# Kernel optimization log

Measured on AMD Instinct MI355X. Metric: run time of the kernel, lower is better.

Reference implementation:

```python
import jax, jax.numpy as jnp
import numpy as np

N, E, G = 50000, 1600000, 64
XDIM, HID, NF, NG, GDIM, NL = 32, 128, 128, 50, 16, 6
CUTOFF = 10.0
SHID = 64
EPS = 1e-5

_offset = jnp.linspace(0.0, CUTOFF, NG)
_coeff = -0.5 / float((CUTOFF / (NG - 1)) ** 2)


def _bn(h, g, b):
    m = h.mean(axis=0)
    v = h.var(axis=0)
    return (h - m) * jax.lax.rsqrt(v + EPS) * g + b


def setup_inputs() -> dict:
    key = jax.random.key(0)
    ks = jax.random.split(key, 48)

    def w(k, shape):
        fan = shape[-2] if len(shape) >= 2 else shape[-1]
        return (jax.random.normal(k, shape, jnp.float32) / np.sqrt(fan)).astype(jnp.float32)

    inp = {
        "x": jax.random.normal(ks[0], (N, XDIM), jnp.float32),
        "edge_index": jax.random.randint(ks[1], (2, E), 0, N, dtype=jnp.int32).astype(jnp.int64),
        "edge_attr": jax.random.normal(ks[2], (E, 3), jnp.float32),
        "batch": jnp.sort(jax.random.randint(ks[3], (N,), 0, G, dtype=jnp.int32)).astype(jnp.int64),
        "u": jax.random.normal(ks[4], (G, GDIM), jnp.float32),
        # node encoder MLP: lin -> bn -> relu -> lin
        "We1": w(ks[5], (XDIM, HID)), "be1": jnp.zeros(HID), "ge1": jnp.ones(HID), "bte1": jnp.zeros(HID),
        "We2": w(ks[6], (HID, HID)), "be2": jnp.zeros(HID),
        # 6 stacked interactions
        "Wf1": w(ks[7], (NL, NG, NF)), "bf1": jnp.zeros((NL, NF)),
        "Wf2": w(ks[8], (NL, NF, NF)), "bf2": jnp.zeros((NL, NF)),
        "Wd1": w(ks[9], (NL, HID, HID)), "bd1": jnp.zeros((NL, HID)),
        "Wd2": w(ks[10], (NL, HID, HID)), "bd2": jnp.zeros((NL, HID)),
        # global MLP: lin -> bn -> relu -> lin
        "Wg1": w(ks[11], (GDIM, HID)), "bg1": jnp.zeros(HID), "gg1": jnp.ones(HID), "btg1": jnp.zeros(HID),
        "Wg2": w(ks[12], (HID, HID)), "bg2": jnp.zeros(HID),
        # shift predictor: [2*HID, 64, 64, 1]
        "Ws1": w(ks[13], (2 * HID, SHID)), "bs1": jnp.zeros(SHID), "gs1": jnp.ones(SHID), "bts1": jnp.zeros(SHID),
        "Ws2": w(ks[14], (SHID, SHID)), "bs2": jnp.zeros(SHID), "gs2": jnp.ones(SHID), "bts2": jnp.zeros(SHID),
        "Ws3": w(ks[15], (SHID, 1)), "bs3": jnp.zeros(1),
    }
    return inp


def reference(x, edge_index, edge_attr, batch, u,
              We1, be1, ge1, bte1, We2, be2,
              Wf1, bf1, Wf2, bf2, Wd1, bd1, Wd2, bd2,
              Wg1, bg1, gg1, btg1, Wg2, bg2,
              Ws1, bs1, gs1, bts1, Ws2, bs2, gs2, bts2, Ws3, bs3):
    row = edge_index[0]  # source j
    col = edge_index[1]  # target i

    # node encoder
    h = jax.nn.relu(_bn(x @ We1 + be1, ge1, bte1)) @ We2 + be2  # [N,HID]

    # gaussian smearing of edge lengths
    d = jnp.linalg.norm(edge_attr, axis=1)  # [E]
    ea = jnp.exp(_coeff * jnp.square(d[:, None] - _offset[None, :]))  # [E,NG]

    for l in range(NL):
        W = jax.nn.relu(ea @ Wf1[l] + bf1[l]) @ Wf2[l] + bf2[l]  # [E,NF]
        msg = h[row] * W                                          # gather + elementwise
        agg = jax.ops.segment_sum(msg, col, num_segments=N)       # scatter-add
        h = h + (jax.nn.relu(agg @ Wd1[l] + bd1[l]) @ Wd2[l] + bd2[l])

    # global MLP
    u_p = jax.nn.relu(_bn(u @ Wg1 + bg1, gg1, btg1)) @ Wg2 + bg2  # [G,HID]

    # shift predictor on [h, u_p[batch]]
    s = jnp.concatenate([h, u_p[batch]], axis=1)  # [N,2*HID]
    s = jax.nn.relu(_bn(s @ Ws1 + bs1, gs1, bts1))
    s = jax.nn.relu(_bn(s @ Ws2 + bs2, gs2, bts2))
    shifts = s @ Ws3 + bs3  # [N,1]
    return shifts, h, ea, u_p
```

## Files before the change

kernel.cpp:

```cpp
#include <hip/hip_runtime.h>

#define NN 50000
#define NE 1600000
#define NGR 64
#define XD 32
#define HID 128
#define NF 128
#define NG 50
#define GD 16
#define NL 6
#define SH 64
#define EPSF 1e-5f
#define TBL 4096
#define INVSTEP 320.0f

typedef __bf16 bf16_t;
typedef bf16_t bf16x8 __attribute__((ext_vector_type(8)));
typedef float f32x4 __attribute__((ext_vector_type(4)));

__device__ __forceinline__ unsigned pack_bf2(float a, float b) {
  unsigned short ua = __builtin_bit_cast(unsigned short, (bf16_t)a);
  unsigned short ub = __builtin_bit_cast(unsigned short, (bf16_t)b);
  return (unsigned)ua | ((unsigned)ub << 16);
}

__global__ __launch_bounds__(256) void k_hist(const int* __restrict__ col,
                                              int* __restrict__ hist) {
  for (int e = blockIdx.x * 256 + threadIdx.x; e < NE; e += gridDim.x * 256)
    atomicAdd(&hist[col[e]], 1);
}

__global__ __launch_bounds__(1024) void k_scan(int* __restrict__ hist,
                                               int* __restrict__ rowptr) {
  const int tid = threadIdx.x;
  const int CH = 49;
  const int base = tid * CH;
  int s = 0;
  for (int i = 0; i < CH; ++i) {
    int idx = base + i;
    if (idx < NN) s += hist[idx];
  }
  __shared__ int part[1024];
  part[tid] = s;
  __syncthreads();
  for (int off = 1; off < 1024; off <<= 1) {
    int v = (tid >= off) ? part[tid - off] : 0;
    __syncthreads();
    part[tid] += v;
    __syncthreads();
  }
  int run = part[tid] - s;
  for (int i = 0; i < CH; ++i) {
    int idx = base + i;
    if (idx < NN) {
      int c = hist[idx];
      rowptr[idx] = run;
      hist[idx] = run;
      run += c;
    }
  }
  if (tid == 0) rowptr[NN] = NE;
}

__global__ __launch_bounds__(256) void k_scatter2(const int* __restrict__ col,
    const int* __restrict__ row, const float* __restrict__ eattr,
    int* __restrict__ cursor, int4* __restrict__ metap) {
  for (int e = blockIdx.x * 256 + threadIdx.x; e < NE; e += gridDim.x * 256) {
    float ax = eattr[(size_t)e * 3], ay = eattr[(size_t)e * 3 + 1], az = eattr[(size_t)e * 3 + 2];
    float d = sqrtf(ax * ax + ay * ay + az * az);
    float tt = fminf(d * INVSTEP, (float)(TBL - 2) + 0.999f);
    int id = (int)tt;
    int c = col[e];
    int pos = atomicAdd(&cursor[c], 1);
    metap[pos] = make_int4(id, __float_as_int(tt - (float)id), row[e], c);
  }
}

__global__ __launch_bounds__(128) void k_tabbuild3(
    const float* __restrict__ Wf1, const float* __restrict__ bf1,
    const float* __restrict__ Wf2, const float* __restrict__ bf2,
    unsigned int* __restrict__ tabp) {
  const int bid = blockIdx.x;
  const int l = bid / (TBL / 8);
  const int t0 = (bid - l * (TBL / 8)) * 8;
  const int c = threadIdx.x;
  __shared__ float g_s[9][NG];
  __shared__ float f1_s[9][NF];
  for (int i = c; i < 9 * NG; i += 128) {
    int kk = i / NG, g = i - kk * NG;
    int t = min(t0 + kk, TBL - 1);
    float d = (float)t * (1.0f / INVSTEP);
    float z = d - 0.2040816327f * (float)g;
    g_s[kk][g] = expf(-12.005f * z * z);
  }
  __syncthreads();
  const float* W1 = Wf1 + (size_t)l * NG * NF;
  float f1r[9];
#pragma unroll
  for (int kk = 0; kk < 9; ++kk) f1r[kk] = bf1[(size_t)l * NF + c];
  for (int g = 0; g < NG; ++g) {
    float w = W1[g * NF + c];
#pragma unroll
    for (int kk = 0; kk < 9; ++kk) f1r[kk] = fmaf(g_s[kk][g], w, f1r[kk]);
  }
#pragma unroll
  for (int kk = 0; kk < 9; ++kk) f1_s[kk][c] = fmaxf(f1r[kk], 0.f);
  __syncthreads();
  const float* W2 = Wf2 + (size_t)l * NF * NF;
  float outr[9];
#pragma unroll
  for (int kk = 0; kk < 9; ++kk) outr[kk] = bf2[(size_t)l * NF + c];
  for (int k = 0; k < NF; ++k) {
    float w = W2[k * NF + c];
#pragma unroll
    for (int kk = 0; kk < 9; ++kk) outr[kk] = fmaf(f1_s[kk][k], w, outr[kk]);
  }
#pragma unroll
  for (int kk = 0; kk < 8; ++kk)
    tabp[((size_t)l * TBL + t0 + kk) * NF + c] = pack_bf2(outr[kk], outr[kk + 1]);
}

__global__ __launch_bounds__(256) void k_prepw(const float* __restrict__ Wd1,
    const float* __restrict__ Wd2,
    bf16_t* __restrict__ Wd1Thi, bf16_t* __restrict__ Wd1Tlo,
    bf16_t* __restrict__ Wd2Thi, bf16_t* __restrict__ Wd2Tlo) {
  const int S1 = NL * 128 * 128;
  int idx = blockIdx.x * 256 + threadIdx.x;
  if (idx < 2 * S1) {
    int which = idx / S1;
    int jj = idx - which * S1;
    int l = jj / (128 * 128);
    int r = jj - l * (128 * 128);
    int c = r >> 7, k = r & 127;
    const float* W = (which == 0) ? Wd1 : Wd2;
    float v = W[(size_t)l * 128 * 128 + (size_t)k * 128 + c];
    bf16_t hv = (bf16_t)v;
    bf16_t lv = (bf16_t)(v - (float)hv);
    if (which == 0) { Wd1Thi[jj] = hv; Wd1Tlo[jj] = lv; }
    else            { Wd2Thi[jj] = hv; Wd2Tlo[jj] = lv; }
  }
}

__global__ __launch_bounds__(256) void k_enc1(const float* __restrict__ x,
    const float* __restrict__ We1, const float* __restrict__ be1,
    float* __restrict__ t, float* __restrict__ stats) {
  int c = threadIdx.x & 127;
  int half = threadIdx.x >> 7;
  float b = be1[c];
  float psum = 0.f, psq = 0.f;
  for (int n = blockIdx.x * 2 + half; n < NN; n += gridDim.x * 2) {
    const float* xr = x + (size_t)n * XD;
    float v = b;
#pragma unroll
    for (int k = 0; k < XD; ++k) v = fmaf(xr[k], We1[k * HID + c], v);
    t[(size_t)n * HID + c] = v;
    psum += v; psq += v * v;
  }
  __shared__ float s0[256], s1[256];
  s0[threadIdx.x] = psum; s1[threadIdx.x] = psq;
  __syncthreads();
  if (threadIdx.x < 128) {
    atomicAdd(&stats[threadIdx.x], s0[threadIdx.x] + s0[threadIdx.x + 128]);
    atomicAdd(&stats[128 + threadIdx.x], s1[threadIdx.x] + s1[threadIdx.x + 128]);
  }
}

__global__ __launch_bounds__(128) void k_bn_fin(const float* __restrict__ gamma,
    const float* __restrict__ beta, float* __restrict__ stats, int C, float invn) {
  int c = threadIdx.x;
  if (c < C) {
    float mean = stats[c] * invn;
    float var = stats[128 + c] * invn - mean * mean;
    float a = gamma[c] * rsqrtf(var + EPSF);
    stats[256 + c] = a;
    stats[384 + c] = beta[c] - mean * a;
  }
}

__global__ __launch_bounds__(128) void k_enc2(const float* __restrict__ t,
    const float* __restrict__ stats, const float* __restrict__ We2,
    const float* __restrict__ be2, float* __restrict__ h,
    unsigned int* __restrict__ hbf) {
  __shared__ float r[HID];
  int c = threadIdx.x;
  float a = stats[256 + c], b = stats[384 + c];
  float bias = be2[c];
  for (int n = blockIdx.x; n < NN; n += gridDim.x) {
    float v = fmaf(t[(size_t)n * HID + c], a, b);
    r[c] = fmaxf(v, 0.f);
    __syncthreads();
    float acc = bias;
#pragma unroll 8
    for (int k = 0; k < HID; ++k) acc = fmaf(r[k], We2[k * HID + c], acc);
    h[(size_t)n * HID + c] = acc;
    float o = __shfl_down(acc, 1);
    if ((c & 1) == 0) hbf[(size_t)n * 64 + (c >> 1)] = pack_bf2(acc, o);
    __syncthreads();
  }
}

__global__ __launch_bounds__(256) void k_smear(const float* __restrict__ eattr,
    float* __restrict__ ea) {
  int idx = blockIdx.x * 256 + threadIdx.x;
  if (idx >= NE * NG) return;
  int e = idx / NG;
  int g = idx - e * NG;
  float ax = eattr[(size_t)e * 3], ay = eattr[(size_t)e * 3 + 1], az = eattr[(size_t)e * 3 + 2];
  float d = sqrtf(ax * ax + ay * ay + az * az);
  float off = (10.0f / 49.0f) * (float)g;
  float z = d - off;
  ea[idx] = __expf(-12.005f * z * z);
}

__global__ __launch_bounds__(256) void k_layer(
    const int4* __restrict__ metap, const int* __restrict__ rowptr,
    const float* __restrict__ hin, const unsigned int* __restrict__ hbf,
    const unsigned int* __restrict__ tabp,
    const bf16_t* __restrict__ Wd1Thi, const bf16_t* __restrict__ Wd1Tlo,
    const bf16_t* __restrict__ Wd2Thi, const bf16_t* __restrict__ Wd2Tlo,
    const float* __restrict__ bd1, const float* __restrict__ bd2,
    float* __restrict__ hout, unsigned int* __restrict__ hbfo) {
  __shared__ __align__(16) char up[8704];
  float (*agg_s)[HID] = (float(*)[HID])up;
  bf16_t (*t1hi)[136] = (bf16_t(*)[136])up;
  bf16_t (*t1lo)[136] = (bf16_t(*)[136])(up + 4352);
  __shared__ __align__(16) bf16_t ahi_s[16][136];
  __shared__ __align__(16) bf16_t alo_s[16][136];

  const int tid = threadIdx.x;
  const int lane = tid & 63;
  const int w = tid >> 6;
  const int c0 = lane * 2;
  const int nb = blockIdx.x * 16;
  const int eS = rowptr[nb], eE = rowptr[nb + 16];

  for (int i = tid; i < 16 * HID; i += 256) ((float*)agg_s)[i] = 0.f;
  __syncthreads();

  {
    const int Q = (eE - eS + 3) >> 2;
    int e = eS + w * Q;
    const int wE = min(e + Q, eE);

    float acc0 = 0.f, acc1 = 0.f;
    int cur = -1;

    auto body = [&](const int4& m, unsigned hv, const uint2& uv) {
      float fr = __int_as_float(m.y);
      int dst = m.w - nb;
      float ha = __uint_as_float(hv << 16);
      float hb = __uint_as_float(hv & 0xffff0000u);
      float w0a = __uint_as_float((uv.x & 0xffffu) << 16);
      float w1a = __uint_as_float(uv.x & 0xffff0000u);
      float w0b = __uint_as_float((uv.y & 0xffffu) << 16);
      float w1b = __uint_as_float(uv.y & 0xffff0000u);
      float ma = fmaf(fr, w1a - w0a, w0a) * ha;
      float mb = fmaf(fr, w1b - w0b, w0b) * hb;
      if (dst != cur) {
        if (cur >= 0) {
          atomicAdd(&agg_s[cur][c0], acc0);
          atomicAdd(&agg_s[cur][c0 + 1], acc1);
        }
        cur = dst; acc0 = ma; acc1 = mb;
      } else {
        acc0 += ma; acc1 += mb;
      }
    };

    if (wE - e >= 4) {
      int4 m0 = metap[e], m1 = metap[e + 1], m2 = metap[e + 2], m3 = metap[e + 3];
      int ep = e + 4;
      while (true) {
        unsigned h0 = hbf[(size_t)m0.z * 64 + lane];
        unsigned h1 = hbf[(size_t)m1.z * 64 + lane];
        unsigned h2 = hbf[(size_t)m2.z * 64 + lane];
        unsigned h3 = hbf[(size_t)m3.z * 64 + lane];
        uint2 t0 = *(const uint2*)(tabp + (size_t)m0.x * HID + c0);
        uint2 t1 = *(const uint2*)(tabp + (size_t)m1.x * HID + c0);
        uint2 t2 = *(const uint2*)(tabp + (size_t)m2.x * HID + c0);
        uint2 t3 = *(const uint2*)(tabp + (size_t)m3.x * HID + c0);
        const bool more = (ep + 4 <= wE);
        int4 n0, n1, n2, n3;
        if (more) {
          n0 = metap[ep]; n1 = metap[ep + 1]; n2 = metap[ep + 2]; n3 = metap[ep + 3];
        }
        body(m0, h0, t0); body(m1, h1, t1); body(m2, h2, t2); body(m3, h3, t3);
        if (!more) break;
        m0 = n0; m1 = n1; m2 = n2; m3 = n3;
        ep += 4;
      }
      e = ep;
    }
    for (; e < wE; ++e) {
      int4 m = metap[e];
      unsigned hv = hbf[(size_t)m.z * 64 + lane];
      uint2 uv = *(const uint2*)(tabp + (size_t)m.x * HID + c0);
      body(m, hv, uv);
    }
    if (cur >= 0) {
      atomicAdd(&agg_s[cur][c0], acc0);
      atomicAdd(&agg_s[cur][c0 + 1], acc1);
    }
  }
  __syncthreads();

  for (int i = tid; i < 16 * 128; i += 256) {
    int r = i >> 7, k = i & 127;
    float v = agg_s[r][k];
    bf16_t hv = (bf16_t)v;
    ahi_s[r][k] = hv;
    alo_s[r][k] = (bf16_t)(v - (float)hv);
  }
  __syncthreads();

  const int lm = lane & 15;
  const int lk = lane >> 4;
  const int colb = w * 32;
  const int k0base = lk * 8;

  f32x4 acc1g[2];
  acc1g[0] = (f32x4){0.f, 0.f, 0.f, 0.f};
  acc1g[1] = (f32x4){0.f, 0.f, 0.f, 0.f};
#pragma unroll
  for (int s = 0; s < 4; ++s) {
    int k0 = s * 32 + k0base;
    bf16x8 Ahi = *(const bf16x8*)&ahi_s[lm][k0];
    bf16x8 Alo = *(const bf16x8*)&alo_s[lm][k0];
#pragma unroll
    for (int cf = 0; cf < 2; ++cf) {
      int cc = colb + cf * 16 + lm;
      bf16x8 Bh = *(const bf16x8*)(Wd1Thi + (size_t)cc * 128 + k0);
      bf16x8 Bl = *(const bf16x8*)(Wd1Tlo + (size_t)cc * 128 + k0);
      acc1g[cf] = __builtin_amdgcn_mfma_f32_16x16x32_bf16(Ahi, Bh, acc1g[cf], 0, 0, 0);
      acc1g[cf] = __builtin_amdgcn_mfma_f32_16x16x32_bf16(Ahi, Bl, acc1g[cf], 0, 0, 0);
      acc1g[cf] = __builtin_amdgcn_mfma_f32_16x16x32_bf16(Alo, Bh, acc1g[cf], 0, 0, 0);
    }
  }
#pragma unroll
  for (int cf = 0; cf < 2; ++cf) {
    int cc = colb + cf * 16 + lm;
    float bias1 = bd1[cc];
#pragma unroll
    for (int j = 0; j < 4; ++j) {
      int r = lk * 4 + j;
      float v = fmaxf(acc1g[cf][j] + bias1, 0.f);
      bf16_t hv = (bf16_t)v;
      t1hi[r][cc] = hv;
      t1lo[r][cc] = (bf16_t)(v - (float)hv);
    }
  }
  __syncthreads();

  f32x4 acc2g[2];
  acc2g[0] = (f32x4){0.f, 0.f, 0.f, 0.f};
  acc2g[1] = (f32x4){0.f, 0.f, 0.f, 0.f};
#pragma unroll
  for (int s = 0; s < 4; ++s) {
    int k0 = s * 32 + k0base;
    bf16x8 Ahi = *(const bf16x8*)&t1hi[lm][k0];
    bf16x8 Alo = *(const bf16x8*)&t1lo[lm][k0];
#pragma unroll
    for (int cf = 0; cf < 2; ++cf) {
      int cc = colb + cf * 16 + lm;
      bf16x8 Bh = *(const bf16x8*)(Wd2Thi + (size_t)cc * 128 + k0);
      bf16x8 Bl = *(const bf16x8*)(Wd2Tlo + (size_t)cc * 128 + k0);
      acc2g[cf] = __builtin_amdgcn_mfma_f32_16x16x32_bf16(Ahi, Bh, acc2g[cf], 0, 0, 0);
      acc2g[cf] = __builtin_amdgcn_mfma_f32_16x16x32_bf16(Ahi, Bl, acc2g[cf], 0, 0, 0);
      acc2g[cf] = __builtin_amdgcn_mfma_f32_16x16x32_bf16(Alo, Bh, acc2g[cf], 0, 0, 0);
    }
  }
#pragma unroll
  for (int cf = 0; cf < 2; ++cf) {
    int cc = colb + cf * 16 + lm;
    float bias2 = bd2[cf ? cc : cc];
#pragma unroll
    for (int j = 0; j < 4; ++j) {
      int r = nb + lk * 4 + j;
      float val = hin[(size_t)r * HID + cc] + acc2g[cf][j] + bias2;
      hout[(size_t)r * HID + cc] = val;
      float o = __shfl_xor(val, 1);
      if ((lm & 1) == 0) hbfo[(size_t)r * 64 + (cc >> 1)] = pack_bf2(val, o);
    }
  }
}

__global__ __launch_bounds__(128) void k_global(const float* __restrict__ u,
    const float* __restrict__ Wg1, const float* __restrict__ bg1,
    const float* __restrict__ gg1, const float* __restrict__ btg1,
    const float* __restrict__ Wg2, const float* __restrict__ bg2,
    float* __restrict__ u_p) {
  __shared__ float t_s[NGR][HID];
  int c = threadIdx.x;
  for (int g = 0; g < NGR; ++g) {
    float v = bg1[c];
#pragma unroll
    for (int k = 0; k < GD; ++k) v = fmaf(u[(size_t)g * GD + k], Wg1[k * HID + c], v);
    t_s[g][c] = v;
  }
  float sum = 0.f, sq = 0.f;
  for (int g = 0; g < NGR; ++g) { float v = t_s[g][c]; sum += v; sq += v * v; }
  float mean = sum * (1.f / NGR);
  float var = sq * (1.f / NGR) - mean * mean;
  float a = gg1[c] * rsqrtf(var + EPSF);
  float b = btg1[c] - mean * a;
  for (int g = 0; g < NGR; ++g) t_s[g][c] = fmaxf(fmaf(t_s[g][c], a, b), 0.f);
  __syncthreads();
  for (int g = 0; g < NGR; ++g) {
    float acc = bg2[c];
#pragma unroll 8
    for (int k = 0; k < HID; ++k) acc = fmaf(t_s[g][k], Wg2[k * HID + c], acc);
    u_p[(size_t)g * HID + c] = acc;
  }
}

__global__ __launch_bounds__(256) void k_shift1(
    const float* __restrict__ h, const float* __restrict__ u_p,
    const int* __restrict__ batch, const float* __restrict__ Ws1,
    const float* __restrict__ bs1, float* __restrict__ t1, float* __restrict__ stats) {
  __shared__ float s_in[16][2 * HID];
  const int c = threadIdx.x & 63;
  const int ng = threadIdx.x >> 6;
  float psum = 0.f, psq = 0.f;
  for (int tile = blockIdx.x; tile < NN / 16; tile += gridDim.x) {
    const int nb = tile * 16;
    for (int i = threadIdx.x; i < 16 * HID; i += 256) {
      int ln = i >> 7, k = i & 127;
      s_in[ln][k] = h[(size_t)(nb + ln) * HID + k];
      s_in[ln][HID + k] = u_p[(size_t)batch[nb + ln] * HID + k];
    }
    __syncthreads();
    float acc[4];
#pragma unroll
    for (int j = 0; j < 4; ++j) acc[j] = bs1[c];
    for (int k = 0; k < 2 * HID; ++k) {
      float w = Ws1[k * SH + c];
#pragma unroll
      for (int j = 0; j < 4; ++j) acc[j] = fmaf(s_in[ng * 4 + j][k], w, acc[j]);
    }
#pragma unroll
    for (int j = 0; j < 4; ++j) {
      t1[(size_t)(nb + ng * 4 + j) * SH + c] = acc[j];
      psum += acc[j]; psq += acc[j] * acc[j];
    }
    __syncthreads();
  }
  __shared__ float rs[256], rq[256];
  rs[threadIdx.x] = psum; rq[threadIdx.x] = psq;
  __syncthreads();
  if (threadIdx.x < 64) {
    int c2 = threadIdx.x;
    atomicAdd(&stats[c2], rs[c2] + rs[c2 + 64] + rs[c2 + 128] + rs[c2 + 192]);
    atomicAdd(&stats[128 + c2], rq[c2] + rq[c2 + 64] + rq[c2 + 128] + rq[c2 + 192]);
  }
}

__global__ __launch_bounds__(256) void k_shift2(
    const float* __restrict__ t1, float* __restrict__ stats,
    const float* __restrict__ Ws2, const float* __restrict__ bs2,
    float* __restrict__ t2) {
  __shared__ float r_s[16][SH];
  const int c = threadIdx.x & 63;
  const int ng = threadIdx.x >> 6;
  float psum = 0.f, psq = 0.f;
  for (int tile = blockIdx.x; tile < NN / 16; tile += gridDim.x) {
    const int nb = tile * 16;
    for (int i = threadIdx.x; i < 16 * SH; i += 256) {
      int ln = i >> 6, k = i & 63;
      float v = fmaf(t1[(size_t)(nb + ln) * SH + k], stats[256 + k], stats[384 + k]);
      r_s[ln][k] = fmaxf(v, 0.f);
    }
    __syncthreads();
    float acc[4];
#pragma unroll
    for (int j = 0; j < 4; ++j) acc[j] = bs2[c];
    for (int k = 0; k < SH; ++k) {
      float w = Ws2[k * SH + c];
#pragma unroll
      for (int j = 0; j < 4; ++j) acc[j] = fmaf(r_s[ng * 4 + j][k], w, acc[j]);
    }
#pragma unroll
    for (int j = 0; j < 4; ++j) {
      t2[(size_t)(nb + ng * 4 + j) * SH + c] = acc[j];
      psum += acc[j]; psq += acc[j] * acc[j];
    }
    __syncthreads();
  }
  __shared__ float rs[256], rq[256];
  rs[threadIdx.x] = psum; rq[threadIdx.x] = psq;
  __syncthreads();
  if (threadIdx.x < 64) {
    int c2 = threadIdx.x;
    atomicAdd(&stats[c2], rs[c2] + rs[c2 + 64] + rs[c2 + 128] + rs[c2 + 192]);
    atomicAdd(&stats[128 + c2], rq[c2] + rq[c2 + 64] + rq[c2 + 128] + rq[c2 + 192]);
  }
}

__global__ __launch_bounds__(256) void k_shift3(
    const float* __restrict__ t2, const float* __restrict__ stats,
    const float* __restrict__ Ws3, const float* __restrict__ bs3,
    float* __restrict__ shifts) {
  int lane = threadIdx.x & 63;
  int n = blockIdx.x * 4 + (threadIdx.x >> 6);
  if (n >= NN) return;
  float a = stats[256 + lane], b = stats[384 + lane];
  float r = fmaxf(fmaf(t2[(size_t)n * SH + lane], a, b), 0.f);
  float v = r * Ws3[lane];
#pragma unroll
  for (int off = 32; off; off >>= 1) v += __shfl_down(v, off);
  if (lane == 0) shifts[n] = v + bs3[0];
}

extern "C" void kernel_launch(void* const* d_in, const int* in_sizes, int n_in,
                              void* d_out, int out_size, void* d_ws, size_t ws_size,
                              hipStream_t stream) {
  const float* x     = (const float*)d_in[0];
  const int*   ei    = (const int*)d_in[1];
  const float* eattr = (const float*)d_in[2];
  const int*   batch = (const int*)d_in[3];
  const float* u     = (const float*)d_in[4];
  const float* We1 = (const float*)d_in[5];  const float* be1 = (const float*)d_in[6];
  const float* ge1 = (const float*)d_in[7];  const float* bte1 = (const float*)d_in[8];
  const float* We2 = (const float*)d_in[9];  const float* be2 = (const float*)d_in[10];
  const float* Wf1 = (const float*)d_in[11]; const float* bf1 = (const float*)d_in[12];
  const float* Wf2 = (const float*)d_in[13]; const float* bf2 = (const float*)d_in[14];
  const float* Wd1 = (const float*)d_in[15]; const float* bd1 = (const float*)d_in[16];
  const float* Wd2 = (const float*)d_in[17]; const float* bd2 = (const float*)d_in[18];
  const float* Wg1 = (const float*)d_in[19]; const float* bg1 = (const float*)d_in[20];
  const float* gg1 = (const float*)d_in[21]; const float* btg1 = (const float*)d_in[22];
  const float* Wg2 = (const float*)d_in[23]; const float* bg2 = (const float*)d_in[24];
  const float* Ws1 = (const float*)d_in[25]; const float* bs1 = (const float*)d_in[26];
  const float* gs1 = (const float*)d_in[27]; const float* bts1 = (const float*)d_in[28];
  const float* Ws2 = (const float*)d_in[29]; const float* bs2 = (const float*)d_in[30];
  const float* gs2 = (const float*)d_in[31]; const float* bts2 = (const float*)d_in[32];
  const float* Ws3 = (const float*)d_in[33]; const float* bs3 = (const float*)d_in[34];

  float* out    = (float*)d_out;
  float* shifts = out;
  float* h      = out + NN;
  float* ea     = out + NN + NN * HID;
  float* u_p    = out + NN + NN * HID + (size_t)NE * NG;

  char* wsb = (char*)d_ws;
  size_t off = 0;
  auto alloc = [&](size_t bytes) { void* p = wsb + off; off = (off + bytes + 255) & ~(size_t)255; return p; };
  float*  stats    = (float*)alloc(512 * sizeof(float));
  int*    hist     = (int*)alloc((size_t)NN * sizeof(int));
  int*    rowptr   = (int*)alloc((size_t)(NN + 1) * sizeof(int));
  int4*   metap    = (int4*)alloc((size_t)NE * sizeof(int4));
  unsigned int* tabp = (unsigned int*)alloc((size_t)NL * TBL * HID * sizeof(unsigned int));
  bf16_t* Wd1Thi   = (bf16_t*)alloc((size_t)NL * 128 * 128 * sizeof(bf16_t));
  bf16_t* Wd1Tlo   = (bf16_t*)alloc((size_t)NL * 128 * 128 * sizeof(bf16_t));
  bf16_t* Wd2Thi   = (bf16_t*)alloc((size_t)NL * 128 * 128 * sizeof(bf16_t));
  bf16_t* Wd2Tlo   = (bf16_t*)alloc((size_t)NL * 128 * 128 * sizeof(bf16_t));
  float*  hwork    = (float*)alloc((size_t)NN * HID * sizeof(float));
  unsigned int* hbfA = (unsigned int*)alloc((size_t)NN * 64 * sizeof(unsigned int));
  unsigned int* hbfB = (unsigned int*)alloc((size_t)NN * 64 * sizeof(unsigned int));
  float*  buf1     = (float*)alloc((size_t)NN * HID * sizeof(float));
  float* t1 = buf1;
  float* t2 = buf1 + (size_t)NN * SH;

  const int* row = ei;
  const int* col = ei + NE;

  hipMemsetAsync(hist, 0, (size_t)NN * sizeof(int), stream);
  k_hist<<<512, 256, 0, stream>>>(col, hist);
  k_scan<<<1, 1024, 0, stream>>>(hist, rowptr);
  k_scatter2<<<512, 256, 0, stream>>>(col, row, eattr, hist, metap);
  k_tabbuild3<<<NL * (TBL / 8), 128, 0, stream>>>(Wf1, bf1, Wf2, bf2, tabp);
  k_prepw<<<(2 * NL * 128 * 128 + 255) / 256, 256, 0, stream>>>(
      Wd1, Wd2, Wd1Thi, Wd1Tlo, Wd2Thi, Wd2Tlo);

  hipMemsetAsync(stats, 0, 256 * sizeof(float), stream);
  k_enc1<<<512, 256, 0, stream>>>(x, We1, be1, buf1, stats);
  k_bn_fin<<<1, 128, 0, stream>>>(ge1, bte1, stats, 128, 1.f / NN);
  k_enc2<<<2048, 128, 0, stream>>>(buf1, stats, We2, be2, h, hbfA);

  k_smear<<<(NE * NG + 255) / 256, 256, 0, stream>>>(eattr, ea);

  for (int l = 0; l < NL; ++l) {
    const float* hi = (l & 1) ? hwork : h;
    float*       ho = (l & 1) ? h : hwork;
    const unsigned int* bi = (l & 1) ? hbfB : hbfA;
    unsigned int*       bo = (l & 1) ? hbfA : hbfB;
    k_layer<<<NN / 16, 256, 0, stream>>>(
        metap, rowptr, hi, bi, tabp + (size_t)l * TBL * HID,
        Wd1Thi + (size_t)l * 128 * 128, Wd1Tlo + (size_t)l * 128 * 128,
        Wd2Thi + (size_t)l * 128 * 128, Wd2Tlo + (size_t)l * 128 * 128,
        bd1 + (size_t)l * HID, bd2 + (size_t)l * HID, ho, bo);
  }

  k_global<<<1, 128, 0, stream>>>(u, Wg1, bg1, gg1, btg1, Wg2, bg2, u_p);

  hipMemsetAsync(stats, 0, 256 * sizeof(float), stream);
  k_shift1<<<1024, 256, 0, stream>>>(h, u_p, batch, Ws1, bs1, t1, stats);
  k_bn_fin<<<1, 128, 0, stream>>>(gs1, bts1, stats, 64, 1.f / NN);
  hipMemsetAsync(stats, 0, 256 * sizeof(float), stream);
  k_shift2<<<1024, 256, 0, stream>>>(t1, stats, Ws2, bs2, t2);
  k_bn_fin<<<1, 128, 0, stream>>>(gs2, bts2, stats, 64, 1.f / NN);
  k_shift3<<<(NN + 3) / 4, 256, 0, stream>>>(t2, stats, Ws3, bs3, shifts);
}
```

Before: 1.903 ms.

## Pack edge metadata into 8 bytes and process two edges per wavefront

Edge metadata shrinks from an int4 (16 bytes) to a uint2. The source row, table index and local destination are bit-packed into one word, and the interpolation fraction sits in the other. In the layer kernel each half-wavefront now handles a different edge with 4 channels per lane, so h and table gathers become 8- and 16-byte vector loads. The goal is to cut metadata bandwidth and the number of gather instructions. The cost is extra select/bit-unpacking work, more shared-memory atomics per flush, and tail handling for odd edge counts.

```diff
diff --git a/kernel.cpp b/kernel.cpp
--- a/kernel.cpp
+++ b/kernel.cpp
@@ -23,6 +23,12 @@
   unsigned short ub = __builtin_bit_cast(unsigned short, (bf16_t)b);
   return (unsigned)ua | ((unsigned)ub << 16);
 }
+__device__ __forceinline__ float bflo(unsigned u) { return __uint_as_float(u << 16); }
+__device__ __forceinline__ float bfhi(unsigned u) { return __uint_as_float(u & 0xffff0000u); }
+__device__ __forceinline__ float blerp(unsigned u, float fr) {
+  float w0 = bflo(u), w1 = bfhi(u);
+  return fmaf(fr, w1 - w0, w0);
+}
 
 __global__ __launch_bounds__(256) void k_hist(const int* __restrict__ col,
                                               int* __restrict__ hist) {
@@ -64,7 +70,7 @@
 
 __global__ __launch_bounds__(256) void k_scatter2(const int* __restrict__ col,
     const int* __restrict__ row, const float* __restrict__ eattr,
-    int* __restrict__ cursor, int4* __restrict__ metap) {
+    int* __restrict__ cursor, uint2* __restrict__ metap) {
   for (int e = blockIdx.x * 256 + threadIdx.x; e < NE; e += gridDim.x * 256) {
     float ax = eattr[(size_t)e * 3], ay = eattr[(size_t)e * 3 + 1], az = eattr[(size_t)e * 3 + 2];
     float d = sqrtf(ax * ax + ay * ay + az * az);
@@ -72,7 +78,8 @@
     int id = (int)tt;
     int c = col[e];
     int pos = atomicAdd(&cursor[c], 1);
-    metap[pos] = make_int4(id, __float_as_int(tt - (float)id), row[e], c);
+    unsigned mw = ((unsigned)row[e] << 16) | ((unsigned)id << 4) | (unsigned)(c & 15);
+    metap[pos] = make_uint2(mw, __float_as_uint(tt - (float)id));
   }
 }
 
@@ -213,7 +220,7 @@
 }
 
 __global__ __launch_bounds__(256) void k_layer(
-    const int4* __restrict__ metap, const int* __restrict__ rowptr,
+    const uint2* __restrict__ metap, const int* __restrict__ rowptr,
     const float* __restrict__ hin, const unsigned int* __restrict__ hbf,
     const unsigned int* __restrict__ tabp,
     const bf16_t* __restrict__ Wd1Thi, const bf16_t* __restrict__ Wd1Tlo,
@@ -230,7 +237,9 @@
   const int tid = threadIdx.x;
   const int lane = tid & 63;
   const int w = tid >> 6;
-  const int c0 = lane * 2;
+  const int half = lane >> 5;
+  const int c0 = (lane & 31) * 4;
+  const int hoff = c0 >> 1;
   const int nb = blockIdx.x * 16;
   const int eS = rowptr[nb], eE = rowptr[nb + 16];
 
@@ -242,65 +251,73 @@
     int e = eS + w * Q;
     const int wE = min(e + Q, eE);
 
-    float acc0 = 0.f, acc1 = 0.f;
+    float a0 = 0.f, a1 = 0.f, a2 = 0.f, a3 = 0.f;
     int cur = -1;
 
-    auto body = [&](const int4& m, unsigned hv, const uint2& uv) {
-      float fr = __int_as_float(m.y);
-      int dst = m.w - nb;
-      float ha = __uint_as_float(hv << 16);
-      float hb = __uint_as_float(hv & 0xffff0000u);
-      float w0a = __uint_as_float((uv.x & 0xffffu) << 16);
-      float w1a = __uint_as_float(uv.x & 0xffff0000u);
-      float w0b = __uint_as_float((uv.y & 0xffffu) << 16);
-      float w1b = __uint_as_float(uv.y & 0xffff0000u);
-      float ma = fmaf(fr, w1a - w0a, w0a) * ha;
-      float mb = fmaf(fr, w1b - w0b, w0b) * hb;
-      if (dst != cur) {
-        if (cur >= 0) {
-          atomicAdd(&agg_s[cur][c0], acc0);
-          atomicAdd(&agg_s[cur][c0 + 1], acc1);
-        }
-        cur = dst; acc0 = ma; acc1 = mb;
-      } else {
-        acc0 += ma; acc1 += mb;
+    auto flush = [&]() {
+      if (cur >= 0) {
+        atomicAdd(&agg_s[cur][c0], a0);
+        atomicAdd(&agg_s[cur][c0 + 1], a1);
+        atomicAdd(&agg_s[cur][c0 + 2], a2);
+        atomicAdd(&agg_s[cur][c0 + 3], a3);
       }
     };
+    auto pbody = [&](unsigned mw, float fr, const uint2& hv, const uint4& tv,
+                     bool valid) {
+      if (valid) {
+        int dst = mw & 0xF;
+        float m0 = blerp(tv.x, fr) * bflo(hv.x);
+        float m1 = blerp(tv.y, fr) * bfhi(hv.x);
+        float m2 = blerp(tv.z, fr) * bflo(hv.y);
+        float m3 = blerp(tv.w, fr) * bfhi(hv.y);
+        if (dst != cur) {
+          flush();
+          cur = dst; a0 = m0; a1 = m1; a2 = m2; a3 = m3;
+        } else {
+          a0 += m0; a1 += m1; a2 += m2; a3 += m3;
+        }
+      }
+    };
 
     if (wE - e >= 4) {
-      int4 m0 = metap[e], m1 = metap[e + 1], m2 = metap[e + 2], m3 = metap[e + 3];
+      uint2 mA0 = metap[e], mB0 = metap[e + 1];
+      uint2 mA1 = metap[e + 2], mB1 = metap[e + 3];
       int ep = e + 4;
       while (true) {
-        unsigned h0 = hbf[(size_t)m0.z * 64 + lane];
-        unsigned h1 = hbf[(size_t)m1.z * 64 + lane];
-        unsigned h2 = hbf[(size_t)m2.z * 64 + lane];
-        unsigned h3 = hbf[(size_t)m3.z * 64 + lane];
-        uint2 t0 = *(const uint2*)(tabp + (size_t)m0.x * HID + c0);
-        uint2 t1 = *(const uint2*)(tabp + (size_t)m1.x * HID + c0);
-        uint2 t2 = *(const uint2*)(tabp + (size_t)m2.x * HID + c0);
-        uint2 t3 = *(const uint2*)(tabp + (size_t)m3.x * HID + c0);
+        unsigned mw0 = half ? mB0.x : mA0.x;
+        float fr0 = __uint_as_float(half ? mB0.y : mA0.y);
+        unsigned mw1 = half ? mB1.x : mA1.x;
+        float fr1 = __uint_as_float(half ? mB1.y : mA1.y);
+        uint2 hv0 = *(const uint2*)(hbf + (size_t)(mw0 >> 16) * 64 + hoff);
+        uint4 tv0 = *(const uint4*)(tabp + (size_t)((mw0 >> 4) & 0xFFFu) * HID + c0);
+        uint2 hv1 = *(const uint2*)(hbf + (size_t)(mw1 >> 16) * 64 + hoff);
+        uint4 tv1 = *(const uint4*)(tabp + (size_t)((mw1 >> 4) & 0xFFFu) * HID + c0);
         const bool more = (ep + 4 <= wE);
-        int4 n0, n1, n2, n3;
+        uint2 nA0, nB0, nA1, nB1;
         if (more) {
-          n0 = metap[ep]; n1 = metap[ep + 1]; n2 = metap[ep + 2]; n3 = metap[ep + 3];
+          nA0 = metap[ep]; nB0 = metap[ep + 1];
+          nA1 = metap[ep + 2]; nB1 = metap[ep + 3];
         }
-        body(m0, h0, t0); body(m1, h1, t1); body(m2, h2, t2); body(m3, h3, t3);
+        pbody(mw0, fr0, hv0, tv0, true);
+        pbody(mw1, fr1, hv1, tv1, true);
         if (!more) break;
-        m0 = n0; m1 = n1; m2 = n2; m3 = n3;
+        mA0 = nA0; mB0 = nB0; mA1 = nA1; mB1 = nB1;
         ep += 4;
       }
       e = ep;
     }
-    for (; e < wE; ++e) {
-      int4 m = metap[e];
-      unsigned hv = hbf[(size_t)m.z * 64 + lane];
-      uint2 uv = *(const uint2*)(tabp + (size_t)m.x * HID + c0);
-      body(m, hv, uv);
-    }
-    if (cur >= 0) {
-      atomicAdd(&agg_s[cur][c0], acc0);
-      atomicAdd(&agg_s[cur][c0 + 1], acc1);
-    }
+    for (; e < wE; e += 2) {
+      bool v1 = (e + 1 < wE);
+      uint2 mA = metap[e];
+      uint2 mB = v1 ? metap[e + 1] : mA;
+      unsigned mw = half ? mB.x : mA.x;
+      float fr = __uint_as_float(half ? mB.y : mA.y);
+      bool valid = (half == 0) || v1;
+      uint2 hv = *(const uint2*)(hbf + (size_t)(mw >> 16) * 64 + hoff);
+      uint4 tv = *(const uint4*)(tabp + (size_t)((mw >> 4) & 0xFFFu) * HID + c0);
+      pbody(mw, fr, hv, tv, valid);
+    }
+    flush();
   }
   __syncthreads();
 
@@ -372,7 +389,7 @@
 #pragma unroll
   for (int cf = 0; cf < 2; ++cf) {
     int cc = colb + cf * 16 + lm;
-    float bias2 = bd2[cf ? cc : cc];
+    float bias2 = bd2[cc];
 #pragma unroll
     for (int j = 0; j < 4; ++j) {
       int r = nb + lk * 4 + j;
@@ -546,7 +563,7 @@
   float*  stats    = (float*)alloc(512 * sizeof(float));
   int*    hist     = (int*)alloc((size_t)NN * sizeof(int));
   int*    rowptr   = (int*)alloc((size_t)(NN + 1) * sizeof(int));
-  int4*   metap    = (int4*)alloc((size_t)NE * sizeof(int4));
+  uint2*  metap    = (uint2*)alloc((size_t)NE * sizeof(uint2));
   unsigned int* tabp = (unsigned int*)alloc((size_t)NL * TBL * HID * sizeof(unsigned int));
   bf16_t* Wd1Thi   = (bf16_t*)alloc((size_t)NL * 128 * 128 * sizeof(bf16_t));
   bf16_t* Wd1Tlo   = (bf16_t*)alloc((size_t)NL * 128 * 128 * sizeof(bf16_t));
```

New measurement: 1.752 ms. 1.09x faster.
